# Optimization experiments

Hardware: AMD Instinct MI355X
Metric: run time of the kernel (lower is better)

## Reference

```python
import jax, jax.numpy as jnp
import numpy as np

IN_F = 4096
OUT_F = 4096
K = 16
THRESH = 0.0


def _group_ids():
    # consecutive chunks of size q = IN_F // K; last chunk absorbs remainder
    q, r = IN_F // K, IN_F % K
    ids = np.concatenate([np.full(q, k, np.int32) for k in range(K - 1)]
                         + [np.full(q + r, K - 1, np.int32)])
    return jnp.asarray(ids)


def setup_inputs() -> dict:
    key = jax.random.key(0)
    k1, k2, k3 = jax.random.split(key, 3)
    bound = 1.0 / np.sqrt(IN_F)
    x = jax.random.normal(k1, (8, 2048, IN_F), dtype=jnp.float32)
    weight = jax.random.uniform(k2, (OUT_F, IN_F), jnp.float32, -bound, bound)
    bias = jax.random.uniform(k3, (OUT_F,), jnp.float32, -bound, bound)
    return {"x": x, "weight": weight, "bias": bias}


def reference(x, weight, bias):
    B, T, F = x.shape
    xf = x.reshape(-1, F)                       # [N, F]
    # sum over output units of W @ x_chunk == colsum(W) . x_chunk
    wsum = jnp.sum(weight, axis=0)              # [F]
    contrib = xf * wsum[None, :]                # [N, F]
    gids = _group_ids()
    # group sums: [K, N] -> [N, K]
    g = jax.ops.segment_sum(contrib.T, gids, num_segments=K).T
    cs = jnp.cumsum(g, axis=1)                  # prefix activations [N, K]
    hit = cs >= THRESH
    idx = jnp.where(jnp.any(hit, axis=1), jnp.argmax(hit, axis=1), K - 1)
    S = jnp.take_along_axis(cs, idx[:, None], axis=1)  # [N, 1] scalar activation
    out = jax.nn.sigmoid(S + bias[None, :])     # [N, OUT_F]
    return out.reshape(B, T, OUT_F)
```

## Files before the change

kernel.cpp:

```cpp
#include <hip/hip_runtime.h>

#define IN_F 4096
#define OUT_F 4096
#define KGRP 16
#define N_ROWS (8 * 2048)
#define RPB 8
#define NBLK (N_ROWS / RPB)
#define WPARTS 32
#define PLAIN_ROWS 8192

typedef float f32x4 __attribute__((ext_vector_type(4)));



__global__ __launch_bounds__(256) void wsum_partial_kernel(const float* __restrict__ w,
                                                           double* __restrict__ partial) {
    const int f = blockIdx.x * 256 + threadIdx.x;
    const int r0 = blockIdx.y * (OUT_F / WPARTS);
    const float* p = w + (size_t)r0 * IN_F + f;
    double s = 0.0;
#pragma unroll 16
    for (int o = 0; o < OUT_F / WPARTS; ++o)
        s += (double)__builtin_nontemporal_load(&p[(size_t)o * IN_F]);
    partial[blockIdx.y * IN_F + f] = s;
}

__global__ __launch_bounds__(256) void wsum_reduce_kernel(const double* __restrict__ partial,
                                                          double* __restrict__ wsum) {
    const int f = blockIdx.x * 256 + threadIdx.x;
    double s = 0.0;
#pragma unroll
    for (int p = 0; p < WPARTS; ++p) s += partial[p * IN_F + f];
    wsum[f] = s;
}

__global__ __launch_bounds__(256) void srow_kernel(const float* __restrict__ x,
                                                   const double* __restrict__ wsum,
                                                   float* __restrict__ S) {
    const int t = threadIdx.x;
    const int lane = t & 63;
    const int wave = t >> 6;
    const int n0 = blockIdx.x * RPB;
    const bool pinned = (n0 < PLAIN_ROWS);

    __shared__ double g[RPB][KGRP];

    double wreg[16];
#pragma unroll
    for (int k = 0; k < 4; ++k) {
        const double* wp = &wsum[4 * (k * 256 + t)];
        double2 w01 = *(const double2*)(wp);
        double2 w23 = *(const double2*)(wp + 2);
        wreg[4 * k + 0] = w01.x; wreg[4 * k + 1] = w01.y;
        wreg[4 * k + 2] = w23.x; wreg[4 * k + 3] = w23.y;
    }

    for (int r = 0; r < RPB; ++r) {
        const f32x4* xr = (const f32x4*)(x + (size_t)(n0 + r) * IN_F);
        double part[4];
        if (pinned) {
#pragma unroll
            for (int k = 0; k < 4; ++k) {
                f32x4 v = xr[k * 256 + t];
                part[k] = (double)v.x * wreg[4 * k + 0] + (double)v.y * wreg[4 * k + 1] +
                          (double)v.z * wreg[4 * k + 2] + (double)v.w * wreg[4 * k + 3];
            }
        } else {
#pragma unroll
            for (int k = 0; k < 4; ++k) {
                f32x4 v = __builtin_nontemporal_load(&xr[k * 256 + t]);
                part[k] = (double)v.x * wreg[4 * k + 0] + (double)v.y * wreg[4 * k + 1] +
                          (double)v.z * wreg[4 * k + 2] + (double)v.w * wreg[4 * k + 3];
            }
        }
        {
            double keep01 = (lane & 1) ? part[1] : part[0];
            double send01 = (lane & 1) ? part[0] : part[1];
            double keep23 = (lane & 1) ? part[3] : part[2];
            double send23 = (lane & 1) ? part[2] : part[3];
            double w01 = keep01 + __shfl_xor(send01, 1, 64);
            double w23 = keep23 + __shfl_xor(send23, 1, 64);
            double keep = (lane & 2) ? w23 : w01;
            double send = (lane & 2) ? w01 : w23;
            double rv = keep + __shfl_xor(send, 2, 64);
#pragma unroll
            for (int off = 4; off <= 32; off <<= 1)
                rv += __shfl_xor(rv, off, 64);
            if (lane < 4) g[r][lane * 4 + wave] = rv;
        }
    }
    __syncthreads();

    if (t < RPB) {
        double cs = 0.0, Sv = 0.0;
        bool found = false;
#pragma unroll
        for (int k = 0; k < KGRP; ++k) {
            cs += g[t][k];
            if (!found && cs >= 0.0) { Sv = cs; found = true; }
        }
        if (!found) Sv = cs;
        S[n0 + t] = (float)Sv;
    }
}

__global__ __launch_bounds__(256) void out_kernel(const float* __restrict__ S,
                                                  const float* __restrict__ bias,
                                                  float* __restrict__ out) {
    const int t = threadIdx.x;
    const int n0 = blockIdx.x * RPB;
    const f32x4* b4 = (const f32x4*)bias;

    f32x4 b[4];
#pragma unroll
    for (int k = 0; k < 4; ++k) b[k] = b4[k * 256 + t];

    for (int r = 0; r < RPB; ++r) {
        const float Sv = S[n0 + r];
        f32x4* o4 = (f32x4*)(out + (size_t)(n0 + r) * OUT_F);
#pragma unroll
        for (int k = 0; k < 4; ++k) {
            f32x4 rr;
            rr.x = __builtin_amdgcn_rcpf(1.0f + __expf(-(Sv + b[k].x)));
            rr.y = __builtin_amdgcn_rcpf(1.0f + __expf(-(Sv + b[k].y)));
            rr.z = __builtin_amdgcn_rcpf(1.0f + __expf(-(Sv + b[k].z)));
            rr.w = __builtin_amdgcn_rcpf(1.0f + __expf(-(Sv + b[k].w)));
            __builtin_nontemporal_store(rr, &o4[k * 256 + t]);
        }
    }
}

extern "C" void kernel_launch(void* const* d_in, const int* in_sizes, int n_in,
                              void* d_out, int out_size, void* d_ws, size_t ws_size,
                              hipStream_t stream) {
    const float* x    = (const float*)d_in[0];
    const float* w    = (const float*)d_in[1];
    const float* bias = (const float*)d_in[2];
    float* out = (float*)d_out;

    char* ws = (char*)d_ws;
    double* wsum    = (double*)(ws);
    float*  S       = (float*)(ws + 32 * 1024);
    double* partial = (double*)(ws + 96 * 1024);

    dim3 g1(IN_F / 256, WPARTS);
    wsum_partial_kernel<<<g1, 256, 0, stream>>>(w, partial);
    wsum_reduce_kernel<<<IN_F / 256, 256, 0, stream>>>(partial, wsum);
    srow_kernel<<<NBLK, 256, 0, stream>>>(x, wsum, S);
    out_kernel<<<NBLK, 256, 0, stream>>>(S, bias, out);
}
```

Before: 118.7 us.

## Fuse all four stages into one cooperative persistent kernel with grid syncs

Replaces the four separate launches (partial wsum, reduce, per-row S, output sigmoid) with a single cooperative kernel of 512 blocks that uses grid.sync between phases. Each block handles 32 rows, so S stays in shared memory and never goes through global memory, and the wsum reduction is done with wave shuffles. This removes launch gaps and the S round trip. In exchange the grid is limited to a co-resident size, which may reduce memory-level parallelism. Grid syncs add barrier cost, and the output phase waits behind a grid-wide barrier. The old four-kernel path is kept as a fallback if the cooperative launch fails.

```diff
diff --git a/kernel.cpp b/kernel.cpp
--- a/kernel.cpp
+++ b/kernel.cpp
@@ -1,17 +1,142 @@
 #include <hip/hip_runtime.h>
+#include <hip/hip_cooperative_groups.h>
+
+namespace cg = cooperative_groups;
 
 #define IN_F 4096
 #define OUT_F 4096
 #define KGRP 16
 #define N_ROWS (8 * 2048)
-#define RPB 8
-#define NBLK (N_ROWS / RPB)
 #define WPARTS 32
+
+#define CBLK 512
+#define RPB_C (N_ROWS / CBLK)
+#define RPB_F 8
+#define NBLK_F (N_ROWS / RPB_F)
 #define PLAIN_ROWS 8192
 
 typedef float f32x4 __attribute__((ext_vector_type(4)));
 
 
+__global__ __launch_bounds__(256, 2) void mega_kernel(const float* __restrict__ x,
+                                                      const float* __restrict__ w,
+                                                      const float* __restrict__ bias,
+                                                      float* __restrict__ out,
+                                                      double* __restrict__ partial,
+                                                      double* __restrict__ wsum) {
+    cg::grid_group grid = cg::this_grid();
+    const int t = threadIdx.x;
+    const int b = blockIdx.x;
+    const int lane = t & 63;
+    const int wave = t >> 6;
+
+    {
+        const int bx = b & 15;
+        const int by = b >> 4;
+        const int f = bx * 256 + t;
+        const float* p = w + (size_t)(by * (OUT_F / WPARTS)) * IN_F + f;
+        double s = 0.0;
+#pragma unroll 16
+        for (int o = 0; o < OUT_F / WPARTS; ++o)
+            s += (double)__builtin_nontemporal_load(&p[(size_t)o * IN_F]);
+        partial[by * IN_F + f] = s;
+    }
+    grid.sync();
+
+    {
+        const int col = b * 8 + (t >> 5);
+        const int p = t & 31;
+        double v = partial[(size_t)p * IN_F + col];
+#pragma unroll
+        for (int off = 16; off > 0; off >>= 1)
+            v += __shfl_xor(v, off, 32);
+        if (p == 0) wsum[col] = v;
+    }
+    grid.sync();
+
+    __shared__ double g[RPB_C][KGRP];
+    __shared__ float sS[RPB_C];
+
+    double wreg[16];
+#pragma unroll
+    for (int k = 0; k < 4; ++k) {
+        const double* wp = &wsum[4 * (k * 256 + t)];
+        double2 w01 = *(const double2*)(wp);
+        double2 w23 = *(const double2*)(wp + 2);
+        wreg[4 * k + 0] = w01.x; wreg[4 * k + 1] = w01.y;
+        wreg[4 * k + 2] = w23.x; wreg[4 * k + 3] = w23.y;
+    }
+    const f32x4* b4 = (const f32x4*)bias;
+    f32x4 bb[4];
+#pragma unroll
+    for (int k = 0; k < 4; ++k) bb[k] = b4[k * 256 + t];
+
+    const int n0 = b * RPB_C;
+    const bool pinned = (b < CBLK / 2);
+
+    for (int r = 0; r < RPB_C; ++r) {
+        const f32x4* xr = (const f32x4*)(x + (size_t)(n0 + r) * IN_F);
+        double part[4];
+        if (pinned) {
+#pragma unroll
+            for (int k = 0; k < 4; ++k) {
+                f32x4 v = xr[k * 256 + t];
+                part[k] = (double)v.x * wreg[4 * k + 0] + (double)v.y * wreg[4 * k + 1] +
+                          (double)v.z * wreg[4 * k + 2] + (double)v.w * wreg[4 * k + 3];
+            }
+        } else {
+#pragma unroll
+            for (int k = 0; k < 4; ++k) {
+                f32x4 v = __builtin_nontemporal_load(&xr[k * 256 + t]);
+                part[k] = (double)v.x * wreg[4 * k + 0] + (double)v.y * wreg[4 * k + 1] +
+                          (double)v.z * wreg[4 * k + 2] + (double)v.w * wreg[4 * k + 3];
+            }
+        }
+        double keep01 = (lane & 1) ? part[1] : part[0];
+        double send01 = (lane & 1) ? part[0] : part[1];
+        double keep23 = (lane & 1) ? part[3] : part[2];
+        double send23 = (lane & 1) ? part[2] : part[3];
+        double w01 = keep01 + __shfl_xor(send01, 1, 64);
+        double w23 = keep23 + __shfl_xor(send23, 1, 64);
+        double keep = (lane & 2) ? w23 : w01;
+        double send = (lane & 2) ? w01 : w23;
+        double rv = keep + __shfl_xor(send, 2, 64);
+#pragma unroll
+        for (int off = 4; off <= 32; off <<= 1)
+            rv += __shfl_xor(rv, off, 64);
+        if (lane < 4) g[r][lane * 4 + wave] = rv;
+    }
+    __syncthreads();
+
+    if (t < RPB_C) {
+        double cs = 0.0, Sv = 0.0;
+        bool found = false;
+#pragma unroll
+        for (int k = 0; k < KGRP; ++k) {
+            cs += g[t][k];
+            if (!found && cs >= 0.0) { Sv = cs; found = true; }
+        }
+        if (!found) Sv = cs;
+        sS[t] = (float)Sv;
+    }
+    __syncthreads();
+
+    grid.sync();
+
+    for (int r = 0; r < RPB_C; ++r) {
+        const float Sv = sS[r];
+        f32x4* o4 = (f32x4*)(out + (size_t)(n0 + r) * OUT_F);
+#pragma unroll
+        for (int k = 0; k < 4; ++k) {
+            f32x4 rr;
+            rr.x = __builtin_amdgcn_rcpf(1.0f + __expf(-(Sv + bb[k].x)));
+            rr.y = __builtin_amdgcn_rcpf(1.0f + __expf(-(Sv + bb[k].y)));
+            rr.z = __builtin_amdgcn_rcpf(1.0f + __expf(-(Sv + bb[k].z)));
+            rr.w = __builtin_amdgcn_rcpf(1.0f + __expf(-(Sv + bb[k].w)));
+            __builtin_nontemporal_store(rr, &o4[k * 256 + t]);
+        }
+    }
+}
 
 __global__ __launch_bounds__(256) void wsum_partial_kernel(const float* __restrict__ w,
                                                            double* __restrict__ partial) {
@@ -40,10 +165,10 @@
     const int t = threadIdx.x;
     const int lane = t & 63;
     const int wave = t >> 6;
-    const int n0 = blockIdx.x * RPB;
+    const int n0 = blockIdx.x * RPB_F;
     const bool pinned = (n0 < PLAIN_ROWS);
 
-    __shared__ double g[RPB][KGRP];
+    __shared__ double g[RPB_F][KGRP];
 
     double wreg[16];
 #pragma unroll
@@ -55,7 +180,7 @@
         wreg[4 * k + 2] = w23.x; wreg[4 * k + 3] = w23.y;
     }
 
-    for (int r = 0; r < RPB; ++r) {
+    for (int r = 0; r < RPB_F; ++r) {
         const f32x4* xr = (const f32x4*)(x + (size_t)(n0 + r) * IN_F);
         double part[4];
         if (pinned) {
@@ -73,25 +198,23 @@
                           (double)v.z * wreg[4 * k + 2] + (double)v.w * wreg[4 * k + 3];
             }
         }
-        {
-            double keep01 = (lane & 1) ? part[1] : part[0];
-            double send01 = (lane & 1) ? part[0] : part[1];
-            double keep23 = (lane & 1) ? part[3] : part[2];
-            double send23 = (lane & 1) ? part[2] : part[3];
-            double w01 = keep01 + __shfl_xor(send01, 1, 64);
-            double w23 = keep23 + __shfl_xor(send23, 1, 64);
-            double keep = (lane & 2) ? w23 : w01;
-            double send = (lane & 2) ? w01 : w23;
-            double rv = keep + __shfl_xor(send, 2, 64);
-#pragma unroll
-            for (int off = 4; off <= 32; off <<= 1)
-                rv += __shfl_xor(rv, off, 64);
-            if (lane < 4) g[r][lane * 4 + wave] = rv;
-        }
+        double keep01 = (lane & 1) ? part[1] : part[0];
+        double send01 = (lane & 1) ? part[0] : part[1];
+        double keep23 = (lane & 1) ? part[3] : part[2];
+        double send23 = (lane & 1) ? part[2] : part[3];
+        double w01 = keep01 + __shfl_xor(send01, 1, 64);
+        double w23 = keep23 + __shfl_xor(send23, 1, 64);
+        double keep = (lane & 2) ? w23 : w01;
+        double send = (lane & 2) ? w01 : w23;
+        double rv = keep + __shfl_xor(send, 2, 64);
+#pragma unroll
+        for (int off = 4; off <= 32; off <<= 1)
+            rv += __shfl_xor(rv, off, 64);
+        if (lane < 4) g[r][lane * 4 + wave] = rv;
     }
     __syncthreads();
 
-    if (t < RPB) {
+    if (t < RPB_F) {
         double cs = 0.0, Sv = 0.0;
         bool found = false;
 #pragma unroll
@@ -108,14 +231,14 @@
                                                   const float* __restrict__ bias,
                                                   float* __restrict__ out) {
     const int t = threadIdx.x;
-    const int n0 = blockIdx.x * RPB;
+    const int n0 = blockIdx.x * RPB_F;
     const f32x4* b4 = (const f32x4*)bias;
 
     f32x4 b[4];
 #pragma unroll
     for (int k = 0; k < 4; ++k) b[k] = b4[k * 256 + t];
 
-    for (int r = 0; r < RPB; ++r) {
+    for (int r = 0; r < RPB_F; ++r) {
         const float Sv = S[n0 + r];
         f32x4* o4 = (f32x4*)(out + (size_t)(n0 + r) * OUT_F);
 #pragma unroll
@@ -143,9 +266,15 @@
     float*  S       = (float*)(ws + 32 * 1024);
     double* partial = (double*)(ws + 96 * 1024);
 
-    dim3 g1(IN_F / 256, WPARTS);
-    wsum_partial_kernel<<<g1, 256, 0, stream>>>(w, partial);
-    wsum_reduce_kernel<<<IN_F / 256, 256, 0, stream>>>(partial, wsum);
-    srow_kernel<<<NBLK, 256, 0, stream>>>(x, wsum, S);
-    out_kernel<<<NBLK, 256, 0, stream>>>(S, bias, out);
-}
+    void* args[] = {(void*)&x, (void*)&w, (void*)&bias, (void*)&out,
+                    (void*)&partial, (void*)&wsum};
+    hipError_t err = hipLaunchCooperativeKernel((void*)mega_kernel, dim3(CBLK),
+                                                dim3(256), args, 0, stream);
+    if (err != hipSuccess) {
+        dim3 g1(IN_F / 256, WPARTS);
+        wsum_partial_kernel<<<g1, 256, 0, stream>>>(w, partial);
+        wsum_reduce_kernel<<<IN_F / 256, 256, 0, stream>>>(partial, wsum);
+        srow_kernel<<<NBLK_F, 256, 0, stream>>>(x, wsum, S);
+        out_kernel<<<NBLK_F, 256, 0, stream>>>(S, bias, out);
+    }
+}
```

New measurement: 296.5 us. 2.5x slower.
